# Performance work log

Hardware: AMD Instinct MI355X
Metric: run time of the kernel (lower is better)

The kernel has to match this reference:

```python
import jax, jax.numpy as jnp
import numpy as np

# Static architecture of the decoded CNN (matches init_kwargs index_dict)
KERNEL_NO = [64, 128, 256]
KERNEL_SIZE = [9, 9, 9]
CH_IN = [3, 64, 128]
IDX_START = [0, 1792, 75648]
I_DIM = 370816  # last slice's last index + 1
D_MODEL = 512
BATCH = 128
N_LAYERS = len(KERNEL_NO)


def _build_slices():
    """Replicates DebedderNeuron.get_kernel_slices(); per-layer int32 index matrix [K_l, L_l]."""
    sl = []
    for idx in range(N_LAYERS):
        rows = []
        for kd in range(KERNEL_NO[idx]):
            s = IDX_START[idx] + kd * KERNEL_SIZE[idx] * CH_IN[idx]
            e = s + KERNEL_SIZE[idx] * CH_IN[idx]
            bias = IDX_START[idx] + KERNEL_NO[idx] * KERNEL_SIZE[idx] * CH_IN[idx] + kd
            ik = list(range(s, e)) + [bias]
            if idx < N_LAYERS - 1:
                for kn in range(KERNEL_NO[idx + 1]):
                    ns = (IDX_START[idx + 1] + kd * KERNEL_SIZE[idx + 1]
                          + kn * CH_IN[idx + 1] * KERNEL_SIZE[idx + 1])
                    ik.extend(range(ns, ns + KERNEL_SIZE[idx + 1]))
            rows.append(ik)
        sl.append(jnp.asarray(np.array(rows, dtype=np.int32)))
    return sl

IDX = _build_slices()  # lengths per row: [1180, 2881, 1153]


def setup_inputs() -> dict:
    key = jax.random.key(0)
    ks = jax.random.split(key, 7)
    dims = [int(IDX[l].shape[1]) for l in range(N_LAYERS)]
    inp = {"x": jax.random.normal(ks[0], (BATCH, sum(KERNEL_NO), D_MODEL), jnp.float32)}
    for l in range(N_LAYERS):
        inp[f"W{l}"] = jax.random.normal(ks[1 + 2 * l], (D_MODEL, dims[l]), jnp.float32) * 0.02
        inp[f"b{l}"] = jax.random.normal(ks[2 + 2 * l], (dims[l],), jnp.float32) * 0.02
    return inp


def reference(x, W0, b0, W1, b1, W2, b2):
    # One shared Linear per CNN layer (as in the torch module); batch all kernels of a
    # layer into a single GEMM, then scatter-add into the flat weight vector y.
    Ws = [W0, W1, W2]
    bs = [b0, b1, b2]
    y = jnp.zeros((x.shape[0], I_DIM), x.dtype)
    off = 0
    for l in range(N_LAYERS):
        K = KERNEL_NO[l]
        yt = jnp.einsum('bkd,di->bki', x[:, off:off + K], Ws[l]) + bs[l]  # [B, K_l, L_l]
        y = y.at[:, IDX[l]].add(yt)  # overlapping scatter-add, matches sequential += in torch
        off += K
    # middle layers are written twice (own slice + previous layer's extension) -> halve
    y = y.at[:, IDX_START[1]:IDX_START[-1]].multiply(0.5)
    return y
```

## Files before the change

### kernel.cpp

```cpp
#include <hip/hip_runtime.h>
#include <cstdint>

typedef short short8 __attribute__((ext_vector_type(8)));
typedef float f32x4 __attribute__((ext_vector_type(4)));

#define LDS_AS3(p) ((__attribute__((address_space(3))) unsigned*)(p))
#define GLB_AS1(p) ((const __attribute__((address_space(1))) unsigned*)(p))

__device__ inline unsigned bfpack(float a, float b) {
    union { float f; unsigned u; } ua, ub;
    ua.f = a; ub.f = b;
    unsigned lo = (ua.u + 0x7FFFu + ((ua.u >> 16) & 1u)) >> 16;
    unsigned hi = (ub.u + 0x7FFFu + ((ub.u >> 16) & 1u)) & 0xFFFF0000u;
    return lo | hi;
}
__device__ inline unsigned short bf16of(float a) { return (unsigned short)bfpack(a, 0.0f); }
__device__ inline float bf2f(unsigned short s) {
    union { unsigned u; float f; } x; x.u = (unsigned)s << 16; return x.f;
}

__global__ __launch_bounds__(256)
void cvt_x(const float* __restrict__ X, unsigned short* __restrict__ XB)
{
    const int g = blockIdx.x * 256 + threadIdx.x;
    const float4 v0 = *(const float4*)(X + (size_t)g * 8);
    const float4 v1 = *(const float4*)(X + (size_t)g * 8 + 4);
    uint4 u;
    u.x = bfpack(v0.x, v0.y); u.y = bfpack(v0.z, v0.w);
    u.z = bfpack(v1.x, v1.y); u.w = bfpack(v1.z, v1.w);
    *(uint4*)(XB + (size_t)g * 8) = u;
}

template <int N>
__global__ __launch_bounds__(256)
void cvt_w(const float* __restrict__ W, unsigned short* __restrict__ WT)
{
    const int g = blockIdx.x * 256 + threadIdx.x;
    if (g >= N * 64) return;
    const int n = g % N, d8 = g / N;
    const float* p = W + (size_t)d8 * 8 * N + n;
    uint4 u;
    u.x = bfpack(p[0],             p[(size_t)N]);
    u.y = bfpack(p[2 * (size_t)N], p[3 * (size_t)N]);
    u.z = bfpack(p[4 * (size_t)N], p[5 * (size_t)N]);
    u.w = bfpack(p[6 * (size_t)N], p[7 * (size_t)N]);
    *(uint4*)(WT + (size_t)n * 512 + d8 * 8) = u;
}

template <int MODE>
__global__ __launch_bounds__(512, 2)
void gemm_pipe(const unsigned short* __restrict__ XB,
               const unsigned short* __restrict__ WT,
               const float* __restrict__ BIAS, float* __restrict__ Y,
               const unsigned short* __restrict__ EXTI,
               unsigned short* __restrict__ EXTO)
{
    constexpr int K_L  = (MODE == 0) ? 64 : (MODE == 1) ? 128 : 256;
    constexpr int LOGK = (MODE == 0) ? 6  : (MODE == 1) ? 7   : 8;
    constexpr int N    = (MODE == 0) ? 1180 : (MODE == 1) ? 2881 : 1153;
    constexpr int XOFF = (MODE == 0) ? 0 : (MODE == 1) ? 64 : 192;
    constexpr int NT   = (N + 127) / 128;

    __shared__ __align__(16) unsigned short lA[3 * 256 * 64];
    __shared__ __align__(16) unsigned short lB[3 * 128 * 64];

    const int t    = threadIdx.x;
    const int lane = t & 63;
    const int wv   = t >> 6;
    const int wr   = wv >> 1;
    const int wn   = wv & 1;
    const int kq   = lane >> 4;
    const int lr16 = lane & 15;

    const int cpx = (int)gridDim.x >> 3;
    const int wg  = (blockIdx.x & 7) * cpx + (blockIdx.x >> 3);
    const int nt  = wg % NT;
    const int mt  = wg / NT;
    const int m0  = mt * 256;
    const int n0  = nt * 128;

    auto stageA = [&](int buf, int kt, int rnd) {
        const int c   = rnd * 512 + t;
        const int row = c >> 3, p = c & 7, l = p ^ (row & 7);
        const int m   = m0 + row;
        const int b   = m >> LOGK, kd = m & (K_L - 1);
        const unsigned short* gp =
            XB + ((size_t)(b * 448 + XOFF + kd) << 9) + kt * 64 + l * 8;
        __builtin_amdgcn_global_load_lds(GLB_AS1(gp),
            LDS_AS3(lA + (size_t)buf * (256 * 64) + c * 8), 16, 0, 0);
    };
    auto stageB = [&](int buf, int kt, int rnd) {
        const int c   = rnd * 512 + t;
        const int row = c >> 3, p = c & 7, l = p ^ (row & 7);
        int gc = n0 + row; if (gc > N - 1) gc = N - 1;
        const unsigned short* gp = WT + (size_t)gc * 512 + kt * 64 + l * 8;
        __builtin_amdgcn_global_load_lds(GLB_AS1(gp),
            LDS_AS3(lB + (size_t)buf * (128 * 64) + c * 8), 16, 0, 0);
    };
    auto stage3 = [&](int buf, int kt, int half) {
        stageA(buf, kt, half * 2);
        stageA(buf, kt, half * 2 + 1);
        stageB(buf, kt, half);
    };

    f32x4 acc[4][4] = {};

    stage3(0, 0, 0); stage3(0, 0, 1);
    stage3(1, 1, 0); stage3(1, 1, 1);

    #pragma unroll 1
    for (int kt = 0; kt < 8; ++kt) {
        const int buf = kt % 3;
        if (kt < 7) asm volatile("s_waitcnt vmcnt(6)" ::: "memory");
        else        asm volatile("s_waitcnt vmcnt(0)" ::: "memory");
        __builtin_amdgcn_s_barrier();

        const unsigned short* Ab = lA + (size_t)buf * (256 * 64);
        const unsigned short* Bb = lB + (size_t)buf * (128 * 64);

        #pragma unroll
        for (int ks = 0; ks < 2; ++ks) {
            const int s = ks * 4 + kq;
            short8 af[4], bf[4];
            #pragma unroll
            for (int mi = 0; mi < 4; ++mi) {
                const int row = wr * 64 + mi * 16 + lr16;
                af[mi] = *(const short8*)(Ab + row * 64 + ((s ^ (row & 7)) * 8));
            }
            #pragma unroll
            for (int ni = 0; ni < 4; ++ni) {
                const int row = wn * 64 + ni * 16 + lr16;
                bf[ni] = *(const short8*)(Bb + row * 64 + ((s ^ (row & 7)) * 8));
            }
            if (kt < 6) stage3((kt + 2) % 3, kt + 2, ks);
            __builtin_amdgcn_s_setprio(1);
            #pragma unroll
            for (int mi = 0; mi < 4; ++mi)
                #pragma unroll
                for (int ni = 0; ni < 4; ++ni)
                    acc[mi][ni] = __builtin_amdgcn_mfma_f32_16x16x32_bf16(
                        af[mi], bf[ni], acc[mi][ni], 0, 0, 0);
            __builtin_amdgcn_s_setprio(0);
        }
    }

    #pragma unroll
    for (int ni = 0; ni < 4; ++ni) {
        const int n = n0 + wn * 64 + ni * 16 + lr16;
        if (n >= N) continue;
        const float bias = BIAS[n];
        #pragma unroll
        for (int mi = 0; mi < 4; ++mi) {
            #pragma unroll
            for (int r = 0; r < 4; ++r) {
                const int m  = m0 + wr * 64 + mi * 16 + kq * 4 + r;
                const int b  = m >> LOGK;
                const int kd = m & (K_L - 1);
                const float v = acc[mi][ni][r] + bias;
                float* yb = Y + (size_t)b * 370816;
                if constexpr (MODE == 0) {
                    if (n < 27)       yb[kd * 27 + n] = v;
                    else if (n == 27) yb[1728 + kd]   = v;
                    else EXTO[((size_t)(b * 64 + kd)) * 1152 + (n - 28)] = bf16of(v);
                } else if constexpr (MODE == 1) {
                    if (n < 576) {
                        const float e = bf2f(EXTI[((size_t)(b * 64 + n / 9)) * 1152 + kd * 9 + n % 9]);
                        yb[1792 + kd * 576 + n] = 0.5f * (v + e);
                    } else if (n == 576) yb[75520 + kd] = 0.5f * v;
                    else EXTO[((size_t)(b * 128 + kd)) * 2304 + (n - 577)] = bf16of(v);
                } else {
                    if (n < 1152) {
                        const float e = bf2f(EXTI[((size_t)(b * 128 + n / 9)) * 2304 + kd * 9 + n % 9]);
                        yb[75648 + kd * 1152 + n] = v + e;
                    } else yb[370560 + kd] = v;
                }
            }
        }
    }
}

extern "C" void kernel_launch(void* const* d_in, const int* in_sizes, int n_in,
                              void* d_out, int out_size, void* d_ws, size_t ws_size,
                              hipStream_t stream)
{
    const float* x  = (const float*)d_in[0];
    const float* W0 = (const float*)d_in[1];
    const float* b0 = (const float*)d_in[2];
    const float* W1 = (const float*)d_in[3];
    const float* b1 = (const float*)d_in[4];
    const float* W2 = (const float*)d_in[5];
    const float* b2 = (const float*)d_in[6];
    float* y = (float*)d_out;

    unsigned short* XB   = (unsigned short*)d_ws;
    unsigned short* WT0  = XB   + (size_t)128 * 448 * 512;
    unsigned short* WT1  = WT0  + (size_t)1180 * 512;
    unsigned short* WT2  = WT1  + (size_t)2881 * 512;
    unsigned short* EXT0 = WT2  + (size_t)1153 * 512;
    unsigned short* EXT1 = EXT0 + (size_t)128 * 64 * 1152;

    cvt_x<<<dim3(14336), 256, 0, stream>>>(x, XB);
    cvt_w<1180><<<dim3((1180 * 64 + 255) / 256), 256, 0, stream>>>(W0, WT0);
    cvt_w<2881><<<dim3((2881 * 64 + 255) / 256), 256, 0, stream>>>(W1, WT1);
    cvt_w<1153><<<dim3((1153 * 64 + 255) / 256), 256, 0, stream>>>(W2, WT2);

    gemm_pipe<0><<<dim3(32 * 10),  512, 0, stream>>>(XB, WT0, b0, y, nullptr, EXT0);
    gemm_pipe<1><<<dim3(64 * 23),  512, 0, stream>>>(XB, WT1, b1, y, EXT0, EXT1);
    gemm_pipe<2><<<dim3(128 * 10), 512, 0, stream>>>(XB, WT2, b2, y, EXT1, nullptr);
}
```

Measured before the change: 321.8 us.

## Enlarge GEMM tiles to 256x256 with 1024-thread blocks and double buffering

Grows the output tile from 256x128 to 256x256 using 16 waves per block, so fewer blocks reload the same X rows. It also swaps the three-stage pipeline with explicit vmcnt waits for a simpler two-buffer scheme that uses __syncthreads. The aim is more data reuse per block and fewer blocks overall. The cost is less latency hiding, since the next stage is issued only one step ahead and a full barrier follows each k-step. Padding waste on the N dimension also grows, and the smaller grids (160, 768 and 640 blocks) may underfill the GPU.

```diff
diff --git a/kernel.cpp b/kernel.cpp
--- a/kernel.cpp
+++ b/kernel.cpp
@@ -48,27 +48,27 @@
 }
 
 template <int MODE>
-__global__ __launch_bounds__(512, 2)
-void gemm_pipe(const unsigned short* __restrict__ XB,
-               const unsigned short* __restrict__ WT,
-               const float* __restrict__ BIAS, float* __restrict__ Y,
-               const unsigned short* __restrict__ EXTI,
-               unsigned short* __restrict__ EXTO)
+__global__ __launch_bounds__(1024, 4)
+void gemm_big(const unsigned short* __restrict__ XB,
+              const unsigned short* __restrict__ WT,
+              const float* __restrict__ BIAS, float* __restrict__ Y,
+              const unsigned short* __restrict__ EXTI,
+              unsigned short* __restrict__ EXTO)
 {
     constexpr int K_L  = (MODE == 0) ? 64 : (MODE == 1) ? 128 : 256;
     constexpr int LOGK = (MODE == 0) ? 6  : (MODE == 1) ? 7   : 8;
     constexpr int N    = (MODE == 0) ? 1180 : (MODE == 1) ? 2881 : 1153;
     constexpr int XOFF = (MODE == 0) ? 0 : (MODE == 1) ? 64 : 192;
-    constexpr int NT   = (N + 127) / 128;
-
-    __shared__ __align__(16) unsigned short lA[3 * 256 * 64];
-    __shared__ __align__(16) unsigned short lB[3 * 128 * 64];
+    constexpr int NT   = (N + 255) / 256;
+
+    __shared__ __align__(16) unsigned short lA[2][256 * 64];
+    __shared__ __align__(16) unsigned short lB[2][256 * 64];
 
     const int t    = threadIdx.x;
     const int lane = t & 63;
     const int wv   = t >> 6;
-    const int wr   = wv >> 1;
-    const int wn   = wv & 1;
+    const int wr   = wv >> 2;
+    const int wc   = wv & 3;
     const int kq   = lane >> 4;
     const int lr16 = lane & 15;
 
@@ -77,46 +77,40 @@
     const int nt  = wg % NT;
     const int mt  = wg / NT;
     const int m0  = mt * 256;
-    const int n0  = nt * 128;
-
-    auto stageA = [&](int buf, int kt, int rnd) {
-        const int c   = rnd * 512 + t;
-        const int row = c >> 3, p = c & 7, l = p ^ (row & 7);
-        const int m   = m0 + row;
-        const int b   = m >> LOGK, kd = m & (K_L - 1);
-        const unsigned short* gp =
-            XB + ((size_t)(b * 448 + XOFF + kd) << 9) + kt * 64 + l * 8;
-        __builtin_amdgcn_global_load_lds(GLB_AS1(gp),
-            LDS_AS3(lA + (size_t)buf * (256 * 64) + c * 8), 16, 0, 0);
+    const int n0  = nt * 256;
+
+    auto stage = [&](int buf, int kt) {
+        #pragma unroll
+        for (int i = 0; i < 2; ++i) {
+            const int c   = i * 1024 + t;
+            const int row = c >> 3, p = c & 7, l = p ^ (row & 7);
+            const int m   = m0 + row;
+            const int b   = m >> LOGK, kd = m & (K_L - 1);
+            const unsigned short* gp =
+                XB + ((size_t)(b * 448 + XOFF + kd) << 9) + kt * 64 + l * 8;
+            __builtin_amdgcn_global_load_lds(GLB_AS1(gp),
+                LDS_AS3(&lA[buf][c * 8]), 16, 0, 0);
+        }
+        #pragma unroll
+        for (int i = 0; i < 2; ++i) {
+            const int c   = i * 1024 + t;
+            const int row = c >> 3, p = c & 7, l = p ^ (row & 7);
+            int gc = n0 + row; if (gc > N - 1) gc = N - 1;
+            const unsigned short* gp = WT + (size_t)gc * 512 + kt * 64 + l * 8;
+            __builtin_amdgcn_global_load_lds(GLB_AS1(gp),
+                LDS_AS3(&lB[buf][c * 8]), 16, 0, 0);
+        }
     };
-    auto stageB = [&](int buf, int kt, int rnd) {
-        const int c   = rnd * 512 + t;
-        const int row = c >> 3, p = c & 7, l = p ^ (row & 7);
-        int gc = n0 + row; if (gc > N - 1) gc = N - 1;
-        const unsigned short* gp = WT + (size_t)gc * 512 + kt * 64 + l * 8;
-        __builtin_amdgcn_global_load_lds(GLB_AS1(gp),
-            LDS_AS3(lB + (size_t)buf * (128 * 64) + c * 8), 16, 0, 0);
-    };
-    auto stage3 = [&](int buf, int kt, int half) {
-        stageA(buf, kt, half * 2);
-        stageA(buf, kt, half * 2 + 1);
-        stageB(buf, kt, half);
-    };
 
     f32x4 acc[4][4] = {};
 
-    stage3(0, 0, 0); stage3(0, 0, 1);
-    stage3(1, 1, 0); stage3(1, 1, 1);
+    stage(0, 0);
+    __syncthreads();
 
     #pragma unroll 1
     for (int kt = 0; kt < 8; ++kt) {
-        const int buf = kt % 3;
-        if (kt < 7) asm volatile("s_waitcnt vmcnt(6)" ::: "memory");
-        else        asm volatile("s_waitcnt vmcnt(0)" ::: "memory");
-        __builtin_amdgcn_s_barrier();
-
-        const unsigned short* Ab = lA + (size_t)buf * (256 * 64);
-        const unsigned short* Bb = lB + (size_t)buf * (128 * 64);
+        const int buf = kt & 1;
+        if (kt < 7) stage(buf ^ 1, kt + 1);
 
         #pragma unroll
         for (int ks = 0; ks < 2; ++ks) {
@@ -125,14 +119,13 @@
             #pragma unroll
             for (int mi = 0; mi < 4; ++mi) {
                 const int row = wr * 64 + mi * 16 + lr16;
-                af[mi] = *(const short8*)(Ab + row * 64 + ((s ^ (row & 7)) * 8));
+                af[mi] = *(const short8*)(&lA[buf][row * 64 + ((s ^ (row & 7)) * 8)]);
             }
             #pragma unroll
             for (int ni = 0; ni < 4; ++ni) {
-                const int row = wn * 64 + ni * 16 + lr16;
-                bf[ni] = *(const short8*)(Bb + row * 64 + ((s ^ (row & 7)) * 8));
+                const int row = wc * 64 + ni * 16 + lr16;
+                bf[ni] = *(const short8*)(&lB[buf][row * 64 + ((s ^ (row & 7)) * 8)]);
             }
-            if (kt < 6) stage3((kt + 2) % 3, kt + 2, ks);
             __builtin_amdgcn_s_setprio(1);
             #pragma unroll
             for (int mi = 0; mi < 4; ++mi)
@@ -142,11 +135,12 @@
                         af[mi], bf[ni], acc[mi][ni], 0, 0, 0);
             __builtin_amdgcn_s_setprio(0);
         }
+        __syncthreads();
     }
 
     #pragma unroll
     for (int ni = 0; ni < 4; ++ni) {
-        const int n = n0 + wn * 64 + ni * 16 + lr16;
+        const int n = n0 + wc * 64 + ni * 16 + lr16;
         if (n >= N) continue;
         const float bias = BIAS[n];
         #pragma unroll
@@ -204,7 +198,7 @@
     cvt_w<2881><<<dim3((2881 * 64 + 255) / 256), 256, 0, stream>>>(W1, WT1);
     cvt_w<1153><<<dim3((1153 * 64 + 255) / 256), 256, 0, stream>>>(W2, WT2);
 
-    gemm_pipe<0><<<dim3(32 * 10),  512, 0, stream>>>(XB, WT0, b0, y, nullptr, EXT0);
-    gemm_pipe<1><<<dim3(64 * 23),  512, 0, stream>>>(XB, WT1, b1, y, EXT0, EXT1);
-    gemm_pipe<2><<<dim3(128 * 10), 512, 0, stream>>>(XB, WT2, b2, y, EXT1, nullptr);
-}
+    gemm_big<0><<<dim3(32 * 5),   1024, 0, stream>>>(XB, WT0, b0, y, nullptr, EXT0);
+    gemm_big<1><<<dim3(64 * 12),  1024, 0, stream>>>(XB, WT1, b1, y, EXT0, EXT1);
+    gemm_big<2><<<dim3(128 * 5),  1024, 0, stream>>>(XB, WT2, b2, y, EXT1, nullptr);
+}
```

Measured after the change: 308.2 us. -4.2%, faster.
